# Optimization experiments

Hardware: AMD Instinct MI355X
Metric: run time of the kernel (lower is better)

## Reference

```python
import jax, jax.numpy as jnp
import numpy as np

D_MODEL, N_HEADS, D_C, D_COMP, D_ROPE = 2048, 16, 512, 768, 64
D_HEAD = D_MODEL // N_HEADS  # 128
B, S = 2, 2048
ROPE_THETA = 10000.0


def _rope_cos_sin(seq_len, dim):
    # frequencies for pairwise complex rotation, dim = per-head rope dim (even)
    inv_freq = 1.0 / (ROPE_THETA ** (jnp.arange(0, dim, 2, dtype=jnp.float32) / dim))
    t = jnp.arange(seq_len, dtype=jnp.float32)
    ang = t[:, None] * inv_freq[None, :]  # [S, dim/2]
    return jnp.cos(ang), jnp.sin(ang)


def _apply_rope(x, cos, sin):
    # x: [B, S, H, dr]; rotate consecutive pairs (view_as_complex semantics)
    x1, x2 = x[..., 0::2], x[..., 1::2]
    c = cos[None, :, None, :]
    s = sin[None, :, None, :]
    y1 = x1 * c - x2 * s
    y2 = x1 * s + x2 * c
    return jnp.stack([y1, y2], axis=-1).reshape(x.shape)


def setup_inputs() -> dict:
    key = jax.random.key(0)
    ks = jax.random.split(key, 9)
    sc = 0.02
    return {
        "x": jax.random.normal(ks[0], (B, S, D_MODEL), jnp.float32),
        "Wd": jax.random.normal(ks[1], (D_MODEL, D_C), jnp.float32) * sc,
        "bd": jnp.zeros((D_C,), jnp.float32),
        "Wu": jax.random.normal(ks[2], (D_C, N_HEADS * D_HEAD), jnp.float32) * sc,
        "bu": jnp.zeros((N_HEADS * D_HEAD,), jnp.float32),
        "Wqd": jax.random.normal(ks[3], (D_MODEL, D_COMP), jnp.float32) * sc,
        "bqd": jnp.zeros((D_COMP,), jnp.float32),
        "Wqu": jax.random.normal(ks[4], (D_COMP, N_HEADS * D_HEAD), jnp.float32) * sc,
        "bqu": jnp.zeros((N_HEADS * D_HEAD,), jnp.float32),
        "Wqr": jax.random.normal(ks[5], (D_COMP, N_HEADS * D_ROPE), jnp.float32) * sc,
        "bqr": jnp.zeros((N_HEADS * D_ROPE,), jnp.float32),
        "Wkr": jax.random.normal(ks[6], (D_MODEL, N_HEADS * D_ROPE), jnp.float32) * sc,
        "bkr": jnp.zeros((N_HEADS * D_ROPE,), jnp.float32),
        "Wo": jax.random.normal(ks[7], (N_HEADS * D_HEAD, D_MODEL), jnp.float32) * sc,
        "bo": jnp.zeros((D_MODEL,), jnp.float32),
    }


def reference(x, Wd, bd, Wu, bu, Wqd, bqd, Wqu, bqu, Wqr, bqr, Wkr, bkr, Wo, bo):
    b, s, _ = x.shape
    # low-rank KV compression
    kv_c = x @ Wd + bd                                   # [B,S,d_c]
    kv_up = (kv_c @ Wu + bu).reshape(b, s, N_HEADS, D_HEAD)  # shared K-content / V
    # low-rank Q compression
    q_cmp = x @ Wqd + bqd                                # [B,S,d_comp]
    q_c = (q_cmp @ Wqu + bqu).reshape(b, s, N_HEADS, D_HEAD)
    # decoupled RoPE branches
    cos, sin = _rope_cos_sin(s, D_ROPE)
    q_r = _apply_rope((q_cmp @ Wqr + bqr).reshape(b, s, N_HEADS, D_ROPE), cos, sin)
    k_r = _apply_rope((x @ Wkr + bkr).reshape(b, s, N_HEADS, D_ROPE), cos, sin)
    q = jnp.concatenate([q_c, q_r], axis=-1)             # [B,S,H,dh+dr]
    k = jnp.concatenate([kv_up, k_r], axis=-1)           # [B,S,H,dh+dr]
    scale = 1.0 / np.sqrt(D_HEAD).astype(np.float32)
    scores = jnp.einsum('bqhd,bkhd->bhqk', q, k) * scale  # [B,H,S,S]
    probs = jax.nn.softmax(scores, axis=-1)
    out = jnp.einsum('bhqk,bkhd->bqhd', probs, kv_up)    # v == kv_up (as in source)
    out = out.reshape(b, s, N_HEADS * D_HEAD)
    return out @ Wo + bo
```

## Files before the change

kernel.cpp:

```cpp
#include <hip/hip_runtime.h>
#include <cmath>

typedef __bf16 bf16;
typedef __bf16 bf16x8 __attribute__((ext_vector_type(8)));
typedef __bf16 bf16x4 __attribute__((ext_vector_type(4)));
typedef __bf16 bf16x2 __attribute__((ext_vector_type(2)));
typedef float f32x4 __attribute__((ext_vector_type(4)));
typedef int i32x4 __attribute__((ext_vector_type(4)));

#define S_LEN 2048
#define QK_LD 3072

__device__ __forceinline__ void async_copy16(const bf16* g, bf16* l) {
    __builtin_amdgcn_global_load_lds(
        (const __attribute__((address_space(1))) void*)g,
        (__attribute__((address_space(3))) void*)l, 16, 0, 0);
}

__device__ __forceinline__ unsigned packbf(float a, float b) {
    bf16x2 v; v[0] = (bf16)a; v[1] = (bf16)b;
    return __builtin_bit_cast(unsigned, v);
}

__global__ __launch_bounds__(256) void cast_f32_bf16(const float* __restrict__ in,
                                                     bf16* __restrict__ out) {
    size_t i = ((size_t)blockIdx.x * 256 + threadIdx.x) * 8;
    float4 a = *(const float4*)(in + i);
    float4 b = *(const float4*)(in + i + 4);
    bf16x8 v;
    v[0] = (bf16)a.x; v[1] = (bf16)a.y; v[2] = (bf16)a.z; v[3] = (bf16)a.w;
    v[4] = (bf16)b.x; v[5] = (bf16)b.y; v[6] = (bf16)b.z; v[7] = (bf16)b.w;
    *(bf16x8*)(out + i) = v;
}

struct TSeg { const float* src; bf16* dst; int K, N, blk0; };
struct TArgs { TSeg s[7]; };

__global__ __launch_bounds__(256) void transpose_all(TArgs a) {
    __shared__ float tile[64][68];
    int b = blockIdx.x, si = 0;
#pragma unroll
    for (int i = 1; i < 7; ++i) if (b >= a.s[i].blk0) si = i;
    TSeg sg = a.s[si];
    int local = b - sg.blk0;
    int kTiles = sg.K >> 6;
    int kt = local % kTiles, nt = local / kTiles;
    int k0 = kt * 64, n0 = nt * 64;
    int K = sg.K, N = sg.N;
    int t = threadIdx.x;
#pragma unroll
    for (int i = 0; i < 4; ++i) {
        int c = t + i * 256;
        int r = c >> 4, off = (c & 15) * 4;
        float4 v = *(const float4*)(sg.src + (size_t)(k0 + r) * N + n0 + off);
        tile[r][off] = v.x; tile[r][off + 1] = v.y;
        tile[r][off + 2] = v.z; tile[r][off + 3] = v.w;
    }
    __syncthreads();
#pragma unroll
    for (int i = 0; i < 2; ++i) {
        int c = t + i * 256;
        int nr = c >> 3, koff = (c & 7) * 8;
        bf16x8 v;
#pragma unroll
        for (int j = 0; j < 8; ++j) v[j] = (bf16)tile[koff + j][nr];
        *(bf16x8*)(sg.dst + (size_t)(n0 + nr) * K + k0 + koff) = v;
    }
}

__global__ __launch_bounds__(256) void setup_small(const float* __restrict__ bd,
                                                   const float* __restrict__ bqd,
                                                   const float* __restrict__ bkr,
                                                   const float* __restrict__ bqu,
                                                   const float* __restrict__ bqr,
                                                   float* __restrict__ bcat,
                                                   float2* __restrict__ tab) {
    if (blockIdx.x < 21) {
        int i = blockIdx.x * 256 + threadIdx.x;
        if (i < 512) bcat[i] = bd[i];
        else if (i < 1280) bcat[i] = bqd[i - 512];
        else if (i < 2304) bcat[i] = bkr[i - 1280];
        else if (i < 4352) bcat[i] = bqu[i - 2304];
        else if (i < 5376) bcat[i] = bqr[i - 4352];
    } else {
        int id = (blockIdx.x - 21) * 256 + threadIdx.x;
        int s = id >> 5, i = id & 31;
        float f = expf(-0.2878231366242557f * (float)i);
        float ang = (float)s * f;
        tab[id] = make_float2(cosf(ang), sinf(ang));
    }
}

__device__ __forceinline__ void gemm_core(const bf16* __restrict__ A, int lda,
                                          const bf16* __restrict__ Bt,
                                          const float* __restrict__ bias,
                                          void* __restrict__ out0,
                                          void* __restrict__ out1,
                                          int Ndim, int Kdim, int mode,
                                          const float2* __restrict__ tab,
                                          int bn, int bm, bf16* As, bf16* Bs) {
    int t = threadIdx.x;
    int w = t >> 6, lane = t & 63;
    int wm = (w >> 1) * 64, wn = (w & 1) * 64;
    int l15 = lane & 15, q4 = lane >> 4;
    f32x4 acc[4][4] = {};

    int lrow = lane >> 2;
    int lcol = (lane & 3) * 8;
    int c0 = w * 2, c1 = w * 2 + 1;
    const bf16* aS0 = A  + (size_t)(bm * 128 + c0 * 16 + lrow) * lda + lcol;
    const bf16* aS1 = A  + (size_t)(bm * 128 + c1 * 16 + lrow) * lda + lcol;
    const bf16* bS0 = Bt + (size_t)(bn * 128 + c0 * 16 + lrow) * Kdim + lcol;
    const bf16* bS1 = Bt + (size_t)(bn * 128 + c1 * 16 + lrow) * Kdim + lcol;
    bf16* aD0 = &As[c0 * 512]; bf16* aD1 = &As[c1 * 512];
    bf16* bD0 = &Bs[c0 * 512]; bf16* bD1 = &Bs[c1 * 512];

    for (int kt = 0; kt < Kdim; kt += 32) {
        async_copy16(aS0 + kt, aD0);
        async_copy16(aS1 + kt, aD1);
        async_copy16(bS0 + kt, bD0);
        async_copy16(bS1 + kt, bD1);
        __syncthreads();
        bf16x8 af[4], bfr[4];
#pragma unroll
        for (int mb = 0; mb < 4; ++mb)
            af[mb] = *(const bf16x8*)&As[(wm + mb * 16 + l15) * 32 + q4 * 8];
#pragma unroll
        for (int nb = 0; nb < 4; ++nb)
            bfr[nb] = *(const bf16x8*)&Bs[(wn + nb * 16 + l15) * 32 + q4 * 8];
#pragma unroll
        for (int mb = 0; mb < 4; ++mb)
#pragma unroll
            for (int nb = 0; nb < 4; ++nb)
                acc[mb][nb] = __builtin_amdgcn_mfma_f32_16x16x32_bf16(
                    af[mb], bfr[nb], acc[mb][nb], 0, 0, 0);
        __syncthreads();
    }

#pragma unroll
    for (int mb = 0; mb < 4; ++mb) {
        int row = bm * 128 + wm + mb * 16 + q4 * 4;
#pragma unroll
        for (int nb = 0; nb < 4; ++nb) {
            int col = bn * 128 + wn + nb * 16 + l15;
            float bv = bias[col];
            if (mode == 1) {
#pragma unroll
                for (int r = 0; r < 4; ++r)
                    ((float*)out0)[(size_t)(row + r) * Ndim + col] = acc[mb][nb][r] + bv;
            } else if (mode == 4) {
                if (col < 1280) {
#pragma unroll
                    for (int r = 0; r < 4; ++r)
                        ((bf16*)out0)[(size_t)(row + r) * 2304 + col] =
                            (bf16)(acc[mb][nb][r] + bv);
                } else {
                    int rel = col - 1280;
                    int hh = rel >> 6, idx = rel & 63, ii = idx >> 1, odd = idx & 1;
#pragma unroll
                    for (int r = 0; r < 4; ++r) {
                        float vv = acc[mb][nb][r] + bv;
                        float pp = __shfl_xor(vv, 1, 64);
                        float2 cs = tab[((row + r) & 2047) * 32 + ii];
                        float o = vv * cs.x + (odd ? pp * cs.y : -pp * cs.y);
                        ((bf16*)out1)[(size_t)(row + r) * QK_LD + hh * 192 + 128 + idx] =
                            (bf16)o;
                    }
                }
            } else if (mode == 5) {
                if (col < 2048) {
                    int hh = col >> 7, dd = col & 127;
#pragma unroll
                    for (int r = 0; r < 4; ++r)
                        ((bf16*)out0)[(size_t)(row + r) * QK_LD + hh * 192 + dd] =
                            (bf16)(acc[mb][nb][r] + bv);
                } else {
                    int rel = col - 2048;
                    int hh = rel >> 6, idx = rel & 63, ii = idx >> 1, odd = idx & 1;
#pragma unroll
                    for (int r = 0; r < 4; ++r) {
                        float vv = acc[mb][nb][r] + bv;
                        float pp = __shfl_xor(vv, 1, 64);
                        float2 cs = tab[((row + r) & 2047) * 32 + ii];
                        float o = vv * cs.x + (odd ? pp * cs.y : -pp * cs.y);
                        ((bf16*)out0)[(size_t)(row + r) * QK_LD + hh * 192 + 128 + idx] =
                            (bf16)o;
                    }
                }
            } else {
                int hh = col >> 7, dd = col & 127;
                bf16x4 pack;
#pragma unroll
                for (int r = 0; r < 4; ++r) {
                    float vv = acc[mb][nb][r] + bv;
                    ((bf16*)out0)[(size_t)(row + r) * QK_LD + hh * 192 + dd] = (bf16)vv;
                    pack[r] = (bf16)vv;
                }
                int bidx = row >> 11, srow = row & 2047;
                *(bf16x4*)((bf16*)out1 +
                           ((size_t)(bidx * 16 + hh) * 128 + dd) * S_LEN + srow) = pack;
            }
        }
    }
}

__global__ __launch_bounds__(256) void gemm_bt(const bf16* __restrict__ A, int lda,
                                               const bf16* __restrict__ Bt,
                                               const float* __restrict__ bias,
                                               void* __restrict__ out0,
                                               void* __restrict__ out1,
                                               int Ndim, int Kdim, int mode,
                                               const float2* __restrict__ tab) {
    __shared__ bf16 As[128 * 32];
    __shared__ bf16 Bs[128 * 32];
    gemm_core(A, lda, Bt, bias, out0, out1, Ndim, Kdim, mode, tab,
              blockIdx.x, blockIdx.y, As, Bs);
}

__global__ __launch_bounds__(256) void gemm_up(const bf16* __restrict__ xproj,
                                               const bf16* __restrict__ WuT,
                                               const float* __restrict__ bu,
                                               void* __restrict__ kbuf,
                                               void* __restrict__ vt,
                                               const bf16* __restrict__ W2T,
                                               const float* __restrict__ bq,
                                               void* __restrict__ qbuf,
                                               const float2* __restrict__ tab) {
    __shared__ bf16 As[128 * 32];
    __shared__ bf16 Bs[128 * 32];
    int bn = blockIdx.x;
    if (bn < 16)
        gemm_core(xproj, 2304, WuT, bu, kbuf, vt, 2048, 512, 6, tab,
                  bn, blockIdx.y, As, Bs);
    else
        gemm_core(xproj + 512, 2304, W2T, bq, qbuf, nullptr, 3072, 768, 5, tab,
                  bn - 16, blockIdx.y, As, Bs);
}

__global__ __launch_bounds__(256, 2) void attn(const bf16* __restrict__ qbuf,
                                               const bf16* __restrict__ kbuf,
                                               const bf16* __restrict__ vt,
                                               bf16* __restrict__ attnout) {
    __shared__ bf16 Ks[2][32 * 192];
    __shared__ bf16 Vs[2][128 * 32];
    int bh = blockIdx.x;
    int qt = blockIdx.y;
    int b = bh >> 4, h = bh & 15;
    int t = threadIdx.x, w = t >> 6, lane = t & 63;
    int l15 = lane & 15, q4 = lane >> 4;
    const float scale = 0.08838834764831845f;

    bf16x8 qf[2][6];
    {
        size_t base = (size_t)(b * S_LEN + qt * 128 + w * 32) * QK_LD + h * 192;
#pragma unroll
        for (int mb = 0; mb < 2; ++mb)
#pragma unroll
            for (int c = 0; c < 6; ++c)
                qf[mb][c] = *(const bf16x8*)(qbuf + base +
                            (size_t)(mb * 16 + l15) * QK_LD + c * 32 + q4 * 8);
    }

    f32x4 oacc[2][8] = {};
    float denom[2] = {0.f, 0.f};
    const bf16* kb_base = kbuf + (size_t)b * S_LEN * QK_LD + h * 192;
    const bf16* vt_base = vt + (size_t)bh * 128 * S_LEN;

    int kg_[3], kl_[3], vg_[2], vl_[2];
#pragma unroll
    for (int i = 0; i < 3; ++i) {
        int c = t + (i << 8);
        int kr = c / 24, u = c % 24;
        kg_[i] = kr * QK_LD + u * 8;
        kl_[i] = kr * 192 + ((u ^ (kr & 7)) << 3);
    }
#pragma unroll
    for (int i = 0; i < 2; ++i) {
        int c = t + (i << 8);
        int vd = c >> 2, u = c & 3;
        vg_[i] = vd * S_LEN + u * 8;
        vl_[i] = vd * 32 + ((u ^ (vd & 3)) << 3);
    }

    int srcA = ((lane & 16) << 1) + l15;
    int srcB = srcA + 16;
    bool hiK = lane >= 32;

    i32x4 kreg[3], vreg[2];
#pragma unroll
    for (int i = 0; i < 3; ++i) kreg[i] = *(const i32x4*)(kb_base + kg_[i]);
#pragma unroll
    for (int i = 0; i < 2; ++i) vreg[i] = *(const i32x4*)(vt_base + vg_[i]);
#pragma unroll
    for (int i = 0; i < 3; ++i) *(i32x4*)&Ks[0][kl_[i]] = kreg[i];
#pragma unroll
    for (int i = 0; i < 2; ++i) *(i32x4*)&Vs[0][vl_[i]] = vreg[i];
    __syncthreads();

    int cur = 0;
    for (int kt = 0; kt < 64; ++kt) {
        if (kt < 63) {
#pragma unroll
            for (int i = 0; i < 3; ++i)
                kreg[i] = *(const i32x4*)(kb_base +
                          (size_t)(kt + 1) * 32 * QK_LD + kg_[i]);
#pragma unroll
            for (int i = 0; i < 2; ++i)
                vreg[i] = *(const i32x4*)(vt_base + (kt + 1) * 32 + vg_[i]);
        }

        f32x4 sacc[2][2] = {};
        __builtin_amdgcn_s_setprio(1);
#pragma unroll
        for (int c = 0; c < 6; ++c) {
#pragma unroll
            for (int nk = 0; nk < 2; ++nk) {
                bf16x8 kb = *(const bf16x8*)&Ks[cur][(nk * 16 + l15) * 192 +
                              (((c * 4 + q4) ^ (l15 & 7)) << 3)];
#pragma unroll
                for (int mb = 0; mb < 2; ++mb)
                    sacc[mb][nk] = __builtin_amdgcn_mfma_f32_16x16x32_bf16(
                        kb, qf[mb][c], sacc[mb][nk], 0, 0, 0);
            }
        }
        __builtin_amdgcn_s_setprio(0);

        bf16x8 paf[2];
#pragma unroll
        for (int mb = 0; mb < 2; ++mb) {
            unsigned pk[2][2];
#pragma unroll
            for (int nk = 0; nk < 2; ++nk) {
                float e[4];
#pragma unroll
                for (int r = 0; r < 4; ++r) {
                    e[r] = __expf(fminf(sacc[mb][nk][r] * scale, 50.0f));
                    denom[mb] += e[r];
                }
                pk[nk][0] = packbf(e[0], e[1]);
                pk[nk][1] = packbf(e[2], e[3]);
            }
            unsigned d[4];
#pragma unroll
            for (int p = 0; p < 4; ++p) {
                int sl = (p & 2) ? srcB : srcA;
                unsigned va = (unsigned)__shfl((int)pk[0][p & 1], sl, 64);
                unsigned vb = (unsigned)__shfl((int)pk[1][p & 1], sl, 64);
                d[p] = hiK ? vb : va;
            }
            i32x4 di;
            di[0] = (int)d[0]; di[1] = (int)d[1];
            di[2] = (int)d[2]; di[3] = (int)d[3];
            paf[mb] = __builtin_bit_cast(bf16x8, di);
        }

        __builtin_amdgcn_s_setprio(1);
#pragma unroll
        for (int nb = 0; nb < 8; ++nb) {
            bf16x8 vb = *(const bf16x8*)&Vs[cur][(nb * 16 + l15) * 32 +
                          ((q4 ^ (l15 & 3)) << 3)];
#pragma unroll
            for (int mb = 0; mb < 2; ++mb)
                oacc[mb][nb] = __builtin_amdgcn_mfma_f32_16x16x32_bf16(
                    paf[mb], vb, oacc[mb][nb], 0, 0, 0);
        }
        __builtin_amdgcn_s_setprio(0);

        if (kt < 63) {
#pragma unroll
            for (int i = 0; i < 3; ++i) *(i32x4*)&Ks[cur ^ 1][kl_[i]] = kreg[i];
#pragma unroll
            for (int i = 0; i < 2; ++i) *(i32x4*)&Vs[cur ^ 1][vl_[i]] = vreg[i];
        }
        __syncthreads();
        cur ^= 1;
    }

#pragma unroll
    for (int mb = 0; mb < 2; ++mb) {
        denom[mb] += __shfl_xor(denom[mb], 16, 64);
        denom[mb] += __shfl_xor(denom[mb], 32, 64);
    }

#pragma unroll
    for (int mb = 0; mb < 2; ++mb)
#pragma unroll
        for (int r = 0; r < 4; ++r) {
            float dv = __shfl(denom[mb], q4 * 4 + r, 64);
            float inv = 1.0f / dv;
            int row = qt * 128 + w * 32 + mb * 16 + q4 * 4 + r;
#pragma unroll
            for (int nb = 0; nb < 8; ++nb) {
                int col = h * 128 + nb * 16 + l15;
                attnout[(size_t)(b * S_LEN + row) * 2048 + col] =
                    (bf16)(oacc[mb][nb][r] * inv);
            }
        }
}

extern "C" void kernel_launch(void* const* d_in, const int* in_sizes, int n_in,
                              void* d_out, int out_size, void* d_ws, size_t ws_size,
                              hipStream_t stream) {
    const float* x   = (const float*)d_in[0];
    const float* Wd  = (const float*)d_in[1];
    const float* bd  = (const float*)d_in[2];
    const float* Wu  = (const float*)d_in[3];
    const float* bu  = (const float*)d_in[4];
    const float* Wqd = (const float*)d_in[5];
    const float* bqd = (const float*)d_in[6];
    const float* Wqu = (const float*)d_in[7];
    const float* bqu = (const float*)d_in[8];
    const float* Wqr = (const float*)d_in[9];
    const float* bqr = (const float*)d_in[10];
    const float* Wkr = (const float*)d_in[11];
    const float* bkr = (const float*)d_in[12];
    const float* Wo  = (const float*)d_in[13];
    const float* bo  = (const float*)d_in[14];
    float* out = (float*)d_out;

    char* p = (char*)d_ws;
    auto alloc = [&](size_t n) { char* r = p; p += (n + 255) & ~(size_t)255; return r; };
    bf16* xb    = (bf16*)alloc((size_t)4096 * 2048 * 2);
    bf16* W1T   = (bf16*)alloc((size_t)2304 * 2048 * 2);
    bf16* W2T   = (bf16*)alloc((size_t)3072 * 768 * 2);
    bf16* WuT   = (bf16*)alloc((size_t)2048 * 512 * 2);
    bf16* WoT   = (bf16*)alloc((size_t)2048 * 2048 * 2);
    bf16* xproj = (bf16*)alloc((size_t)4096 * 2304 * 2);
    bf16* qbuf  = (bf16*)alloc((size_t)4096 * 3072 * 2);
    bf16* kbuf  = (bf16*)alloc((size_t)4096 * 3072 * 2);
    bf16* vt    = (bf16*)alloc((size_t)32 * 128 * 2048 * 2);
    bf16* aout  = (bf16*)alloc((size_t)4096 * 2048 * 2);
    float* bcat = (float*)alloc((size_t)5376 * 4);
    float2* tab = (float2*)alloc((size_t)65536 * 8);

    cast_f32_bf16<<<dim3(4096), dim3(256), 0, stream>>>(x, xb);

    TArgs ta;
    ta.s[0] = {Wd,  W1T,                       2048, 512,  0};
    ta.s[1] = {Wqd, W1T + (size_t)512 * 2048,  2048, 768,  256};
    ta.s[2] = {Wkr, W1T + (size_t)1280 * 2048, 2048, 1024, 640};
    ta.s[3] = {Wqu, W2T,                       768,  2048, 1152};
    ta.s[4] = {Wqr, W2T + (size_t)2048 * 768,  768,  1024, 1536};
    ta.s[5] = {Wu,  WuT,                       512,  2048, 1728};
    ta.s[6] = {Wo,  WoT,                       2048, 2048, 1984};
    transpose_all<<<dim3(3008), dim3(256), 0, stream>>>(ta);
    setup_small<<<dim3(277), dim3(256), 0, stream>>>(bd, bqd, bkr, bqu, bqr, bcat, tab);

    gemm_bt<<<dim3(18, 32), dim3(256), 0, stream>>>(xb, 2048, W1T, bcat,
                                                    xproj, kbuf, 2304, 2048, 4, tab);
    gemm_up<<<dim3(40, 32), dim3(256), 0, stream>>>(xproj, WuT, bu, kbuf, vt,
                                                    W2T, bcat + 2304, qbuf, tab);

    attn<<<dim3(32, 16), dim3(256), 0, stream>>>(qbuf, kbuf, vt, aout);

    gemm_bt<<<dim3(16, 32), dim3(256), 0, stream>>>(aout, 2048, WoT, bo,
                                                    out, nullptr, 2048, 2048, 1, tab);
}
```

Before: 435.3 us.

## Split attention query tile across eight waves of sixteen rows each

The attention kernel now launches 512 threads per block, and each wave owns 16 query rows instead of 32. This halves the per-wave accumulator and Q-fragment registers, which allows higher occupancy (launch bounds 512,4). The cooperative K/V tile loads are redistributed over the larger block. Each wave now reuses every K/V LDS fragment for half as many MFMAs, so LDS read traffic per FLOP doubles and there are more waves taking part in each barrier.

```diff
diff --git a/kernel.cpp b/kernel.cpp
--- a/kernel.cpp
+++ b/kernel.cpp
@@ -237,7 +237,7 @@
                   bn - 16, blockIdx.y, As, Bs);
 }
 
-__global__ __launch_bounds__(256, 2) void attn(const bf16* __restrict__ qbuf,
+__global__ __launch_bounds__(512, 4) void attn(const bf16* __restrict__ qbuf,
                                                const bf16* __restrict__ kbuf,
                                                const bf16* __restrict__ vt,
                                                bf16* __restrict__ attnout) {
@@ -250,66 +250,63 @@
     int l15 = lane & 15, q4 = lane >> 4;
     const float scale = 0.08838834764831845f;
 
-    bf16x8 qf[2][6];
+    bf16x8 qf[6];
     {
-        size_t base = (size_t)(b * S_LEN + qt * 128 + w * 32) * QK_LD + h * 192;
-#pragma unroll
-        for (int mb = 0; mb < 2; ++mb)
-#pragma unroll
-            for (int c = 0; c < 6; ++c)
-                qf[mb][c] = *(const bf16x8*)(qbuf + base +
-                            (size_t)(mb * 16 + l15) * QK_LD + c * 32 + q4 * 8);
-    }
-
-    f32x4 oacc[2][8] = {};
-    float denom[2] = {0.f, 0.f};
+        size_t base = (size_t)(b * S_LEN + qt * 128 + w * 16 + l15) * QK_LD + h * 192;
+#pragma unroll
+        for (int c = 0; c < 6; ++c)
+            qf[c] = *(const bf16x8*)(qbuf + base + c * 32 + q4 * 8);
+    }
+
+    f32x4 oacc[8] = {};
+    float denom = 0.f;
     const bf16* kb_base = kbuf + (size_t)b * S_LEN * QK_LD + h * 192;
     const bf16* vt_base = vt + (size_t)bh * 128 * S_LEN;
 
-    int kg_[3], kl_[3], vg_[2], vl_[2];
-#pragma unroll
-    for (int i = 0; i < 3; ++i) {
-        int c = t + (i << 8);
+    int kg0, kl0, kg1, kl1, vg0, vl0;
+    {
+        int c = t;
         int kr = c / 24, u = c % 24;
-        kg_[i] = kr * QK_LD + u * 8;
-        kl_[i] = kr * 192 + ((u ^ (kr & 7)) << 3);
-    }
-#pragma unroll
-    for (int i = 0; i < 2; ++i) {
-        int c = t + (i << 8);
+        kg0 = kr * QK_LD + u * 8;
+        kl0 = kr * 192 + ((u ^ (kr & 7)) << 3);
+    }
+    {
+        int c = t + 512;
+        int kr = c / 24, u = c % 24;
+        kg1 = kr * QK_LD + u * 8;
+        kl1 = kr * 192 + ((u ^ (kr & 7)) << 3);
+    }
+    {
+        int c = t;
         int vd = c >> 2, u = c & 3;
-        vg_[i] = vd * S_LEN + u * 8;
-        vl_[i] = vd * 32 + ((u ^ (vd & 3)) << 3);
-    }
+        vg0 = vd * S_LEN + u * 8;
+        vl0 = vd * 32 + ((u ^ (vd & 3)) << 3);
+    }
+    bool kx = (t < 256);
 
     int srcA = ((lane & 16) << 1) + l15;
     int srcB = srcA + 16;
     bool hiK = lane >= 32;
 
-    i32x4 kreg[3], vreg[2];
-#pragma unroll
-    for (int i = 0; i < 3; ++i) kreg[i] = *(const i32x4*)(kb_base + kg_[i]);
-#pragma unroll
-    for (int i = 0; i < 2; ++i) vreg[i] = *(const i32x4*)(vt_base + vg_[i]);
-#pragma unroll
-    for (int i = 0; i < 3; ++i) *(i32x4*)&Ks[0][kl_[i]] = kreg[i];
-#pragma unroll
-    for (int i = 0; i < 2; ++i) *(i32x4*)&Vs[0][vl_[i]] = vreg[i];
+    i32x4 kreg0, kreg1, vreg0;
+    kreg0 = *(const i32x4*)(kb_base + kg0);
+    if (kx) kreg1 = *(const i32x4*)(kb_base + kg1);
+    vreg0 = *(const i32x4*)(vt_base + vg0);
+    *(i32x4*)&Ks[0][kl0] = kreg0;
+    if (kx) *(i32x4*)&Ks[0][kl1] = kreg1;
+    *(i32x4*)&Vs[0][vl0] = vreg0;
     __syncthreads();
 
     int cur = 0;
     for (int kt = 0; kt < 64; ++kt) {
         if (kt < 63) {
-#pragma unroll
-            for (int i = 0; i < 3; ++i)
-                kreg[i] = *(const i32x4*)(kb_base +
-                          (size_t)(kt + 1) * 32 * QK_LD + kg_[i]);
-#pragma unroll
-            for (int i = 0; i < 2; ++i)
-                vreg[i] = *(const i32x4*)(vt_base + (kt + 1) * 32 + vg_[i]);
-        }
-
-        f32x4 sacc[2][2] = {};
+            const bf16* kb = kb_base + (size_t)(kt + 1) * 32 * QK_LD;
+            kreg0 = *(const i32x4*)(kb + kg0);
+            if (kx) kreg1 = *(const i32x4*)(kb + kg1);
+            vreg0 = *(const i32x4*)(vt_base + (kt + 1) * 32 + vg0);
+        }
+
+        f32x4 sacc[2] = {};
         __builtin_amdgcn_s_setprio(1);
 #pragma unroll
         for (int c = 0; c < 6; ++c) {
@@ -317,29 +314,26 @@
             for (int nk = 0; nk < 2; ++nk) {
                 bf16x8 kb = *(const bf16x8*)&Ks[cur][(nk * 16 + l15) * 192 +
                               (((c * 4 + q4) ^ (l15 & 7)) << 3)];
-#pragma unroll
-                for (int mb = 0; mb < 2; ++mb)
-                    sacc[mb][nk] = __builtin_amdgcn_mfma_f32_16x16x32_bf16(
-                        kb, qf[mb][c], sacc[mb][nk], 0, 0, 0);
+                sacc[nk] = __builtin_amdgcn_mfma_f32_16x16x32_bf16(
+                    kb, qf[c], sacc[nk], 0, 0, 0);
             }
         }
         __builtin_amdgcn_s_setprio(0);
 
-        bf16x8 paf[2];
-#pragma unroll
-        for (int mb = 0; mb < 2; ++mb) {
-            unsigned pk[2][2];
-#pragma unroll
-            for (int nk = 0; nk < 2; ++nk) {
-                float e[4];
-#pragma unroll
-                for (int r = 0; r < 4; ++r) {
-                    e[r] = __expf(fminf(sacc[mb][nk][r] * scale, 50.0f));
-                    denom[mb] += e[r];
-                }
-                pk[nk][0] = packbf(e[0], e[1]);
-                pk[nk][1] = packbf(e[2], e[3]);
+        unsigned pk[2][2];
+#pragma unroll
+        for (int nk = 0; nk < 2; ++nk) {
+            float e[4];
+#pragma unroll
+            for (int r = 0; r < 4; ++r) {
+                e[r] = __expf(fminf(sacc[nk][r] * scale, 50.0f));
+                denom += e[r];
             }
+            pk[nk][0] = packbf(e[0], e[1]);
+            pk[nk][1] = packbf(e[2], e[3]);
+        }
+        bf16x8 paf;
+        {
             unsigned d[4];
 #pragma unroll
             for (int p = 0; p < 4; ++p) {
@@ -351,7 +345,7 @@
             i32x4 di;
             di[0] = (int)d[0]; di[1] = (int)d[1];
             di[2] = (int)d[2]; di[3] = (int)d[3];
-            paf[mb] = __builtin_bit_cast(bf16x8, di);
+            paf = __builtin_bit_cast(bf16x8, di);
         }
 
         __builtin_amdgcn_s_setprio(1);
@@ -359,43 +353,35 @@
         for (int nb = 0; nb < 8; ++nb) {
             bf16x8 vb = *(const bf16x8*)&Vs[cur][(nb * 16 + l15) * 32 +
                           ((q4 ^ (l15 & 3)) << 3)];
-#pragma unroll
-            for (int mb = 0; mb < 2; ++mb)
-                oacc[mb][nb] = __builtin_amdgcn_mfma_f32_16x16x32_bf16(
-                    paf[mb], vb, oacc[mb][nb], 0, 0, 0);
+            oacc[nb] = __builtin_amdgcn_mfma_f32_16x16x32_bf16(
+                paf, vb, oacc[nb], 0, 0, 0);
         }
         __builtin_amdgcn_s_setprio(0);
 
         if (kt < 63) {
-#pragma unroll
-            for (int i = 0; i < 3; ++i) *(i32x4*)&Ks[cur ^ 1][kl_[i]] = kreg[i];
-#pragma unroll
-            for (int i = 0; i < 2; ++i) *(i32x4*)&Vs[cur ^ 1][vl_[i]] = vreg[i];
+            *(i32x4*)&Ks[cur ^ 1][kl0] = kreg0;
+            if (kx) *(i32x4*)&Ks[cur ^ 1][kl1] = kreg1;
+            *(i32x4*)&Vs[cur ^ 1][vl0] = vreg0;
         }
         __syncthreads();
         cur ^= 1;
     }
 
-#pragma unroll
-    for (int mb = 0; mb < 2; ++mb) {
-        denom[mb] += __shfl_xor(denom[mb], 16, 64);
-        denom[mb] += __shfl_xor(denom[mb], 32, 64);
-    }
-
-#pragma unroll
-    for (int mb = 0; mb < 2; ++mb)
-#pragma unroll
-        for (int r = 0; r < 4; ++r) {
-            float dv = __shfl(denom[mb], q4 * 4 + r, 64);
-            float inv = 1.0f / dv;
-            int row = qt * 128 + w * 32 + mb * 16 + q4 * 4 + r;
-#pragma unroll
-            for (int nb = 0; nb < 8; ++nb) {
-                int col = h * 128 + nb * 16 + l15;
-                attnout[(size_t)(b * S_LEN + row) * 2048 + col] =
-                    (bf16)(oacc[mb][nb][r] * inv);
-            }
-        }
+    denom += __shfl_xor(denom, 16, 64);
+    denom += __shfl_xor(denom, 32, 64);
+
+#pragma unroll
+    for (int r = 0; r < 4; ++r) {
+        float dv = __shfl(denom, q4 * 4 + r, 64);
+        float inv = 1.0f / dv;
+        int row = qt * 128 + w * 16 + q4 * 4 + r;
+#pragma unroll
+        for (int nb = 0; nb < 8; ++nb) {
+            int col = h * 128 + nb * 16 + l15;
+            attnout[(size_t)(b * S_LEN + row) * 2048 + col] =
+                (bf16)(oacc[nb][r] * inv);
+        }
+    }
 }
 
 extern "C" void kernel_launch(void* const* d_in, const int* in_sizes, int n_in,
@@ -451,7 +437,7 @@
     gemm_up<<<dim3(40, 32), dim3(256), 0, stream>>>(xproj, WuT, bu, kbuf, vt,
                                                     W2T, bcat + 2304, qbuf, tab);
 
-    attn<<<dim3(32, 16), dim3(256), 0, stream>>>(qbuf, kbuf, vt, aout);
+    attn<<<dim3(32, 16), dim3(512), 0, stream>>>(qbuf, kbuf, vt, aout);
 
     gemm_bt<<<dim3(16, 32), dim3(256), 0, stream>>>(aout, 2048, WoT, bo,
                                                     out, nullptr, 2048, 2048, 1, tab);
```

Measured after the change: 439.4 us. About the same (+0.9%).

## Switch attention to 32x32x16 MFMA with 256-row query tiles per block

Applied to the files above, without the earlier changes.

The attention kernel moves from 16x16x32 MFMA to 32x32x16 MFMA. Each wave now covers 64 query rows, so each block handles 256 rows and the grid shrinks from 16 to 8 query tiles. The K and V shared-memory layouts get a new 8-byte-granular swizzle, and the P-fragment shuffle becomes a single xor-32 exchange. The aim is to reuse each K/V tile across twice as many queries and cut LDS traffic and shuffles, but it needs more registers, drops to one block per CU (launch bounds 256,1), and launches only 256 blocks.

```diff
diff --git a/kernel.cpp b/kernel.cpp
--- a/kernel.cpp
+++ b/kernel.cpp
@@ -6,7 +6,9 @@
 typedef __bf16 bf16x4 __attribute__((ext_vector_type(4)));
 typedef __bf16 bf16x2 __attribute__((ext_vector_type(2)));
 typedef float f32x4 __attribute__((ext_vector_type(4)));
+typedef float f32x16 __attribute__((ext_vector_type(16)));
 typedef int i32x4 __attribute__((ext_vector_type(4)));
+typedef int i32x2 __attribute__((ext_vector_type(2)));
 
 #define S_LEN 2048
 #define QK_LD 3072
@@ -237,7 +239,7 @@
                   bn - 16, blockIdx.y, As, Bs);
 }
 
-__global__ __launch_bounds__(256, 2) void attn(const bf16* __restrict__ qbuf,
+__global__ __launch_bounds__(256, 1) void attn(const bf16* __restrict__ qbuf,
                                                const bf16* __restrict__ kbuf,
                                                const bf16* __restrict__ vt,
                                                bf16* __restrict__ attnout) {
@@ -247,44 +249,50 @@
     int qt = blockIdx.y;
     int b = bh >> 4, h = bh & 15;
     int t = threadIdx.x, w = t >> 6, lane = t & 63;
-    int l15 = lane & 15, q4 = lane >> 4;
+    int l31 = lane & 31, hl = lane >> 5;
     const float scale = 0.08838834764831845f;
 
-    bf16x8 qf[2][6];
-    {
-        size_t base = (size_t)(b * S_LEN + qt * 128 + w * 32) * QK_LD + h * 192;
-#pragma unroll
-        for (int mb = 0; mb < 2; ++mb)
-#pragma unroll
-            for (int c = 0; c < 6; ++c)
-                qf[mb][c] = *(const bf16x8*)(qbuf + base +
-                            (size_t)(mb * 16 + l15) * QK_LD + c * 32 + q4 * 8);
-    }
-
-    f32x4 oacc[2][8] = {};
+    bf16x8 qf[2][12];
+#pragma unroll
+    for (int qg = 0; qg < 2; ++qg) {
+        size_t rbase = (size_t)(b * S_LEN + qt * 256 + w * 64 + qg * 32 + l31) * QK_LD
+                       + h * 192 + hl * 8;
+#pragma unroll
+        for (int c = 0; c < 12; ++c)
+            qf[qg][c] = *(const bf16x8*)(qbuf + rbase + c * 16);
+    }
+
+    f32x16 oacc[2][4] = {};
     float denom[2] = {0.f, 0.f};
     const bf16* kb_base = kbuf + (size_t)b * S_LEN * QK_LD + h * 192;
     const bf16* vt_base = vt + (size_t)bh * 128 * S_LEN;
 
-    int kg_[3], kl_[3], vg_[2], vl_[2];
+    int kg_[3], klA_[3], klB_[3];
 #pragma unroll
     for (int i = 0; i < 3; ++i) {
         int c = t + (i << 8);
         int kr = c / 24, u = c % 24;
         kg_[i] = kr * QK_LD + u * 8;
-        kl_[i] = kr * 192 + ((u ^ (kr & 7)) << 3);
-    }
+        int m = kr & 15;
+        klA_[i] = kr * 192 + (((2 * u) ^ m) << 2);
+        klB_[i] = kr * 192 + (((2 * u + 1) ^ m) << 2);
+    }
+    int vg_[2], vlA_[2], vlB_[2];
 #pragma unroll
     for (int i = 0; i < 2; ++i) {
         int c = t + (i << 8);
         int vd = c >> 2, u = c & 3;
         vg_[i] = vd * S_LEN + u * 8;
-        vl_[i] = vd * 32 + ((u ^ (vd & 3)) << 3);
-    }
-
-    int srcA = ((lane & 16) << 1) + l15;
-    int srcB = srcA + 16;
-    bool hiK = lane >= 32;
+        int line = vd >> 1, lm = line & 15;
+        int sl = 8 * (vd & 1) + 2 * u;
+        vlA_[i] = line * 64 + ((sl ^ lm) << 2);
+        vlB_[i] = line * 64 + (((sl + 1) ^ lm) << 2);
+    }
+
+    int mK = l31 & 15;
+    int kRow = l31 * 192;
+    int vLM = l31 >> 1;
+    int vSlotB = 8 * (l31 & 1) + 2 * hl;
 
     i32x4 kreg[3], vreg[2];
 #pragma unroll
@@ -292,108 +300,123 @@
 #pragma unroll
     for (int i = 0; i < 2; ++i) vreg[i] = *(const i32x4*)(vt_base + vg_[i]);
 #pragma unroll
-    for (int i = 0; i < 3; ++i) *(i32x4*)&Ks[0][kl_[i]] = kreg[i];
-#pragma unroll
-    for (int i = 0; i < 2; ++i) *(i32x4*)&Vs[0][vl_[i]] = vreg[i];
+    for (int i = 0; i < 3; ++i) {
+        i32x2 lo; lo[0] = kreg[i][0]; lo[1] = kreg[i][1];
+        i32x2 hi; hi[0] = kreg[i][2]; hi[1] = kreg[i][3];
+        *(i32x2*)&Ks[0][klA_[i]] = lo;
+        *(i32x2*)&Ks[0][klB_[i]] = hi;
+    }
+#pragma unroll
+    for (int i = 0; i < 2; ++i) {
+        i32x2 lo; lo[0] = vreg[i][0]; lo[1] = vreg[i][1];
+        i32x2 hi; hi[0] = vreg[i][2]; hi[1] = vreg[i][3];
+        *(i32x2*)&Vs[0][vlA_[i]] = lo;
+        *(i32x2*)&Vs[0][vlB_[i]] = hi;
+    }
     __syncthreads();
 
     int cur = 0;
     for (int kt = 0; kt < 64; ++kt) {
         if (kt < 63) {
-#pragma unroll
-            for (int i = 0; i < 3; ++i)
-                kreg[i] = *(const i32x4*)(kb_base +
-                          (size_t)(kt + 1) * 32 * QK_LD + kg_[i]);
+            const bf16* kb = kb_base + (size_t)(kt + 1) * 32 * QK_LD;
+#pragma unroll
+            for (int i = 0; i < 3; ++i) kreg[i] = *(const i32x4*)(kb + kg_[i]);
 #pragma unroll
             for (int i = 0; i < 2; ++i)
                 vreg[i] = *(const i32x4*)(vt_base + (kt + 1) * 32 + vg_[i]);
         }
 
-        f32x4 sacc[2][2] = {};
-        __builtin_amdgcn_s_setprio(1);
-#pragma unroll
-        for (int c = 0; c < 6; ++c) {
-#pragma unroll
-            for (int nk = 0; nk < 2; ++nk) {
-                bf16x8 kb = *(const bf16x8*)&Ks[cur][(nk * 16 + l15) * 192 +
-                              (((c * 4 + q4) ^ (l15 & 7)) << 3)];
-#pragma unroll
-                for (int mb = 0; mb < 2; ++mb)
-                    sacc[mb][nk] = __builtin_amdgcn_mfma_f32_16x16x32_bf16(
-                        kb, qf[mb][c], sacc[mb][nk], 0, 0, 0);
-            }
-        }
-        __builtin_amdgcn_s_setprio(0);
-
-        bf16x8 paf[2];
-#pragma unroll
-        for (int mb = 0; mb < 2; ++mb) {
-            unsigned pk[2][2];
-#pragma unroll
-            for (int nk = 0; nk < 2; ++nk) {
-                float e[4];
-#pragma unroll
-                for (int r = 0; r < 4; ++r) {
-                    e[r] = __expf(fminf(sacc[mb][nk][r] * scale, 50.0f));
-                    denom[mb] += e[r];
-                }
-                pk[nk][0] = packbf(e[0], e[1]);
-                pk[nk][1] = packbf(e[2], e[3]);
-            }
-            unsigned d[4];
-#pragma unroll
-            for (int p = 0; p < 4; ++p) {
-                int sl = (p & 2) ? srcB : srcA;
-                unsigned va = (unsigned)__shfl((int)pk[0][p & 1], sl, 64);
-                unsigned vb = (unsigned)__shfl((int)pk[1][p & 1], sl, 64);
-                d[p] = hiK ? vb : va;
-            }
-            i32x4 di;
-            di[0] = (int)d[0]; di[1] = (int)d[1];
-            di[2] = (int)d[2]; di[3] = (int)d[3];
-            paf[mb] = __builtin_bit_cast(bf16x8, di);
-        }
-
-        __builtin_amdgcn_s_setprio(1);
-#pragma unroll
-        for (int nb = 0; nb < 8; ++nb) {
-            bf16x8 vb = *(const bf16x8*)&Vs[cur][(nb * 16 + l15) * 32 +
-                          ((q4 ^ (l15 & 3)) << 3)];
-#pragma unroll
-            for (int mb = 0; mb < 2; ++mb)
-                oacc[mb][nb] = __builtin_amdgcn_mfma_f32_16x16x32_bf16(
-                    paf[mb], vb, oacc[mb][nb], 0, 0, 0);
-        }
-        __builtin_amdgcn_s_setprio(0);
+        f32x16 sacc[2] = {};
+#pragma unroll
+        for (int c = 0; c < 12; ++c) {
+            int u0 = 4 * c + 2 * hl;
+            i32x2 lo = *(const i32x2*)&Ks[cur][kRow + ((u0 ^ mK) << 2)];
+            i32x2 hi = *(const i32x2*)&Ks[cur][kRow + (((u0 + 1) ^ mK) << 2)];
+            i32x4 kv; kv[0] = lo[0]; kv[1] = lo[1]; kv[2] = hi[0]; kv[3] = hi[1];
+            bf16x8 kb = __builtin_bit_cast(bf16x8, kv);
+            sacc[0] = __builtin_amdgcn_mfma_f32_32x32x16_bf16(kb, qf[0][c], sacc[0], 0, 0, 0);
+            sacc[1] = __builtin_amdgcn_mfma_f32_32x32x16_bf16(kb, qf[1][c], sacc[1], 0, 0, 0);
+        }
+
+        bf16x8 paf[2][2];
+#pragma unroll
+        for (int qg = 0; qg < 2; ++qg) {
+            unsigned W[8], pw[8];
+#pragma unroll
+            for (int m = 0; m < 8; ++m) {
+                float e0 = __expf(fminf(sacc[qg][2 * m] * scale, 50.0f));
+                float e1 = __expf(fminf(sacc[qg][2 * m + 1] * scale, 50.0f));
+                denom[qg] += e0 + e1;
+                W[m] = packbf(e0, e1);
+            }
+#pragma unroll
+            for (int m = 0; m < 8; ++m)
+                pw[m] = (unsigned)__shfl_xor((int)W[m], 32, 64);
+#pragma unroll
+            for (int s = 0; s < 2; ++s) {
+                unsigned A = hl ? pw[4 * s + 2] : W[4 * s + 0];
+                unsigned B = hl ? pw[4 * s + 3] : W[4 * s + 1];
+                unsigned C = hl ? W[4 * s + 2] : pw[4 * s + 0];
+                unsigned D = hl ? W[4 * s + 3] : pw[4 * s + 1];
+                i32x4 di; di[0] = (int)A; di[1] = (int)B; di[2] = (int)C; di[3] = (int)D;
+                paf[qg][s] = __builtin_bit_cast(bf16x8, di);
+            }
+        }
+
+#pragma unroll
+        for (int dg = 0; dg < 4; ++dg) {
+#pragma unroll
+            for (int s = 0; s < 2; ++s) {
+                int line = dg * 16 + (l31 >> 1);
+                int s0 = (vSlotB + 4 * s) ^ vLM;
+                int s1 = (vSlotB + 4 * s + 1) ^ vLM;
+                i32x2 lo = *(const i32x2*)&Vs[cur][line * 64 + (s0 << 2)];
+                i32x2 hi = *(const i32x2*)&Vs[cur][line * 64 + (s1 << 2)];
+                i32x4 vv; vv[0] = lo[0]; vv[1] = lo[1]; vv[2] = hi[0]; vv[3] = hi[1];
+                bf16x8 vb = __builtin_bit_cast(bf16x8, vv);
+                oacc[0][dg] = __builtin_amdgcn_mfma_f32_32x32x16_bf16(
+                    paf[0][s], vb, oacc[0][dg], 0, 0, 0);
+                oacc[1][dg] = __builtin_amdgcn_mfma_f32_32x32x16_bf16(
+                    paf[1][s], vb, oacc[1][dg], 0, 0, 0);
+            }
+        }
 
         if (kt < 63) {
 #pragma unroll
-            for (int i = 0; i < 3; ++i) *(i32x4*)&Ks[cur ^ 1][kl_[i]] = kreg[i];
-#pragma unroll
-            for (int i = 0; i < 2; ++i) *(i32x4*)&Vs[cur ^ 1][vl_[i]] = vreg[i];
+            for (int i = 0; i < 3; ++i) {
+                i32x2 lo; lo[0] = kreg[i][0]; lo[1] = kreg[i][1];
+                i32x2 hi; hi[0] = kreg[i][2]; hi[1] = kreg[i][3];
+                *(i32x2*)&Ks[cur ^ 1][klA_[i]] = lo;
+                *(i32x2*)&Ks[cur ^ 1][klB_[i]] = hi;
+            }
+#pragma unroll
+            for (int i = 0; i < 2; ++i) {
+                i32x2 lo; lo[0] = vreg[i][0]; lo[1] = vreg[i][1];
+                i32x2 hi; hi[0] = vreg[i][2]; hi[1] = vreg[i][3];
+                *(i32x2*)&Vs[cur ^ 1][vlA_[i]] = lo;
+                *(i32x2*)&Vs[cur ^ 1][vlB_[i]] = hi;
+            }
         }
         __syncthreads();
         cur ^= 1;
     }
 
-#pragma unroll
-    for (int mb = 0; mb < 2; ++mb) {
-        denom[mb] += __shfl_xor(denom[mb], 16, 64);
-        denom[mb] += __shfl_xor(denom[mb], 32, 64);
-    }
-
-#pragma unroll
-    for (int mb = 0; mb < 2; ++mb)
-#pragma unroll
-        for (int r = 0; r < 4; ++r) {
-            float dv = __shfl(denom[mb], q4 * 4 + r, 64);
+    denom[0] += __shfl_xor(denom[0], 32, 64);
+    denom[1] += __shfl_xor(denom[1], 32, 64);
+
+#pragma unroll
+    for (int qg = 0; qg < 2; ++qg)
+#pragma unroll
+        for (int r = 0; r < 16; ++r) {
+            int rowl = (r & 3) + 8 * (r >> 2) + 4 * hl;
+            float dv = __shfl(denom[qg], rowl, 64);
             float inv = 1.0f / dv;
-            int row = qt * 128 + w * 32 + mb * 16 + q4 * 4 + r;
-#pragma unroll
-            for (int nb = 0; nb < 8; ++nb) {
-                int col = h * 128 + nb * 16 + l15;
+            int row = qt * 256 + w * 64 + qg * 32 + rowl;
+#pragma unroll
+            for (int dg = 0; dg < 4; ++dg) {
+                int col = h * 128 + dg * 32 + l31;
                 attnout[(size_t)(b * S_LEN + row) * 2048 + col] =
-                    (bf16)(oacc[mb][nb][r] * inv);
+                    (bf16)(oacc[qg][dg][r] * inv);
             }
         }
 }
@@ -451,7 +474,7 @@
     gemm_up<<<dim3(40, 32), dim3(256), 0, stream>>>(xproj, WuT, bu, kbuf, vt,
                                                     W2T, bcat + 2304, qbuf, tab);
 
-    attn<<<dim3(32, 16), dim3(256), 0, stream>>>(qbuf, kbuf, vt, aout);
+    attn<<<dim3(32, 8), dim3(256), 0, stream>>>(qbuf, kbuf, vt, aout);
 
     gemm_bt<<<dim3(16, 32), dim3(256), 0, stream>>>(aout, 2048, WoT, bo,
                                                     out, nullptr, 2048, 2048, 1, tab);
```

New measurement: 465.0 us. 6.8% more time.
